# Optimization experiments

Measured on AMD Instinct MI355X. Metric: run time of the kernel, lower is better.

## Reference

```python
import jax, jax.numpy as jnp
import numpy as np

N = 100000      # num_nodes
E = 1600000     # num_edges (avg degree 16)
IN = 128        # in_channels
HID = 8         # hidden_channels (per head)
HEADS = 8
OUT = 64        # out_channels
NEG_SLOPE = 0.2


def setup_inputs() -> dict:
    key = jax.random.key(0)
    ks = jax.random.split(key, 11)
    s = 0.05
    return {
        "x": jax.random.normal(ks[0], (N, IN), jnp.float32),
        "edge_index": jax.random.randint(ks[1], (2, E), 0, N, dtype=jnp.int32),
        "W1": jax.random.normal(ks[2], (IN, HEADS * HID), jnp.float32) * s,
        "a_src1": jax.random.normal(ks[3], (HEADS, HID), jnp.float32) * s,
        "a_dst1": jax.random.normal(ks[4], (HEADS, HID), jnp.float32) * s,
        "b1": jnp.zeros((HEADS * HID,), jnp.float32),
        "W2": jax.random.normal(ks[5], (HEADS * HID, OUT), jnp.float32) * s,
        "a_src2": jax.random.normal(ks[6], (1, OUT), jnp.float32) * s,
        "a_dst2": jax.random.normal(ks[7], (1, OUT), jnp.float32) * s,
        "b2": jnp.zeros((OUT,), jnp.float32),
    }


def gat_conv(x, src, dst, W, a_src, a_dst, bias, heads, out_ch):
    """PyG GATConv (concat=True, dropout=0, self-loops already in src/dst)."""
    n = x.shape[0]
    h = (x @ W).reshape(n, heads, out_ch)               # [N, H, C]
    al_src = jnp.einsum('nhc,hc->nh', h, a_src)          # [N, H]
    al_dst = jnp.einsum('nhc,hc->nh', h, a_dst)          # [N, H]
    e = jax.nn.leaky_relu(al_src[src] + al_dst[dst], NEG_SLOPE)  # [E, H]
    # segment softmax over destination nodes (numerically stable)
    e_max = jax.ops.segment_max(e, dst, num_segments=n)  # [N, H]
    ex = jnp.exp(e - e_max[dst])
    denom = jax.ops.segment_sum(ex, dst, num_segments=n)
    alpha = ex / (denom[dst] + 1e-16)                    # [E, H]
    msg = h[src] * alpha[:, :, None]                     # [E, H, C]
    out = jax.ops.segment_sum(msg, dst, num_segments=n)  # [N, H, C]
    return out.reshape(n, heads * out_ch) + bias


def reference(x, edge_index, W1, a_src1, a_dst1, b1, W2, a_src2, a_dst2, b2):
    n = x.shape[0]
    loops = jnp.arange(n, dtype=edge_index.dtype)
    src = jnp.concatenate([edge_index[0], loops])        # add self-loops (PyG default)
    dst = jnp.concatenate([edge_index[1], loops])
    h = gat_conv(x, src, dst, W1, a_src1, a_dst1, b1, HEADS, HID)
    h = jax.nn.elu(h)
    out = gat_conv(h, src, dst, W2, a_src2, a_dst2, b2, 1, OUT)
    return out
```

## Files before the change

kernel.cpp:

```cpp
#include <hip/hip_runtime.h>
#include <hip/hip_bf16.h>

#define IN_CH   128
#define HEADS   8
#define HID     8
#define MID_CH  64
#define OUT_CH  64
#define CAP     64
#define NRANGE  8
#define NFILLB  256

typedef unsigned short u16;
__device__ __forceinline__ u16 f2bu(float f) {
    union { float f; unsigned int i; } v; v.f = f;
    unsigned int lsb = (v.i >> 16) & 1u;
    return (u16)((v.i + 0x7fffu + lsb) >> 16);
}
__device__ __forceinline__ float2 up2(unsigned int u) {
    union { unsigned int i; float f; } a, b;
    a.i = u << 16; b.i = u & 0xffff0000u;
    return make_float2(a.f, b.f);
}
__device__ __forceinline__ float lrelu(float e) { return (e > 0.f) ? e : 0.2f * e; }

#define FILL_ISSUE(U, D4, S4, P4)                                              \
    do {                                                                        \
        int range_ = (U) & (NRANGE - 1);                                        \
        int chunk_ = (U) >> 3;                                                  \
        int lo_ = (int)(((long long)N * range_) >> 3);                          \
        int hi_ = (int)(((long long)N * (range_ + 1)) >> 3);                    \
        int base_ = (chunk_ * 256 + threadIdx.x) * 4;                           \
        if (base_ + 3 < E) {                                                    \
            D4 = *(const int4*)(dst + base_);                                   \
            bool ix_ = (D4.x >= lo_ && D4.x < hi_);                             \
            bool iy_ = (D4.y >= lo_ && D4.y < hi_);                             \
            bool iz_ = (D4.z >= lo_ && D4.z < hi_);                             \
            bool iw_ = (D4.w >= lo_ && D4.w < hi_);                             \
            if (ix_ | iy_ | iz_ | iw_) {                                        \
                S4 = *(const int4*)(src + base_);                               \
                if (ix_) P4.x = atomicAdd(&deg[D4.x], 1);                       \
                if (iy_) P4.y = atomicAdd(&deg[D4.y], 1);                       \
                if (iz_) P4.z = atomicAdd(&deg[D4.z], 1);                       \
                if (iw_) P4.w = atomicAdd(&deg[D4.w], 1);                       \
            }                                                                   \
        } else {                                                                \
            for (int j_ = 0; j_ < 4; j_++) {                                    \
                int e_ = base_ + j_;                                            \
                if (e_ < E) {                                                   \
                    int d_ = dst[e_];                                           \
                    if (d_ >= lo_ && d_ < hi_) {                                \
                        int p_ = atomicAdd(&deg[d_], 1);                        \
                        if (p_ < CAP) adj[(size_t)d_ * CAP + p_] = src[e_];     \
                    }                                                           \
                }                                                               \
            }                                                                   \
        }                                                                       \
    } while (0)

#define FILL_STORE(D4, S4, P4)                                                  \
    do {                                                                        \
        if (P4.x < CAP) adj[(size_t)D4.x * CAP + P4.x] = S4.x;                  \
        if (P4.y < CAP) adj[(size_t)D4.y * CAP + P4.y] = S4.y;                  \
        if (P4.z < CAP) adj[(size_t)D4.z * CAP + P4.z] = S4.z;                  \
        if (P4.w < CAP) adj[(size_t)D4.w * CAP + P4.w] = S4.w;                  \
    } while (0)

__global__ __launch_bounds__(256, 4) void k12_roles(
    const int* __restrict__ src, const int* __restrict__ dst,
    int* __restrict__ deg, int* __restrict__ adj,
    const float* __restrict__ x, const float* __restrict__ W1,
    const float* __restrict__ a_src, const float* __restrict__ a_dst,
    u16* __restrict__ h1b, float* __restrict__ als, float* __restrict__ ald,
    int E, int N)
{
    __shared__ float Wl[IN_CH * MID_CH];
    __shared__ float xl[16 * IN_CH];
    int bid = blockIdx.x;
    int tid = threadIdx.x;

    if (bid < NFILLB) {
        int range = bid & 7;
        int cstart = bid >> 3;
        int chunks = (E + 1023) >> 10;
        for (int c = cstart; c < chunks; c += 128) {
            int4 dA = make_int4(0,0,0,0), sA = make_int4(0,0,0,0);
            int4 pA = make_int4(CAP,CAP,CAP,CAP);
            int4 dB = make_int4(0,0,0,0), sB = make_int4(0,0,0,0);
            int4 pB = make_int4(CAP,CAP,CAP,CAP);
            int4 dC = make_int4(0,0,0,0), sC = make_int4(0,0,0,0);
            int4 pC = make_int4(CAP,CAP,CAP,CAP);
            int4 dD = make_int4(0,0,0,0), sD = make_int4(0,0,0,0);
            int4 pD = make_int4(CAP,CAP,CAP,CAP);
            FILL_ISSUE(c * 8 + range, dA, sA, pA);
            if (c +  32 < chunks) { int u_ = (c +  32) * 8 + range; FILL_ISSUE(u_, dB, sB, pB); }
            if (c +  64 < chunks) { int u_ = (c +  64) * 8 + range; FILL_ISSUE(u_, dC, sC, pC); }
            if (c +  96 < chunks) { int u_ = (c +  96) * 8 + range; FILL_ISSUE(u_, dD, sD, pD); }
            FILL_STORE(dA, sA, pA);
            FILL_STORE(dB, sB, pB);
            FILL_STORE(dC, sC, pC);
            FILL_STORE(dD, sD, pD);
        }
        return;
    }

    int gid = bid - NFILLB;
    {
        const float4* W4 = (const float4*)W1;
        float4* Wl4 = (float4*)Wl;
        #pragma unroll
        for (int i = tid; i < IN_CH * MID_CH / 4; i += 256) Wl4[i] = W4[i];
    }
    int base = gid * 16;
    {
        float4* xl4 = (float4*)xl;
        const float4* x4 = (const float4*)x;
        #pragma unroll
        for (int i = tid; i < 16 * IN_CH / 4; i += 256) {
            int r = i >> 5;
            int n = base + r;
            xl4[i] = (n < N) ? x4[(size_t)n * (IN_CH / 4) + (i & 31)]
                             : make_float4(0.f, 0.f, 0.f, 0.f);
        }
    }
    __syncthreads();

    int wave = tid >> 6, lane = tid & 63;
    int r0 = wave * 4;
    const float* xr0 = &xl[(r0 + 0) * IN_CH];
    const float* xr1 = &xl[(r0 + 1) * IN_CH];
    const float* xr2 = &xl[(r0 + 2) * IN_CH];
    const float* xr3 = &xl[(r0 + 3) * IN_CH];
    float acc0 = 0.f, acc1 = 0.f, acc2 = 0.f, acc3 = 0.f;
    #pragma unroll 8
    for (int kc = 0; kc < IN_CH; kc += 4) {
        float4 xa = *(const float4*)(xr0 + kc);
        float4 xb = *(const float4*)(xr1 + kc);
        float4 xc = *(const float4*)(xr2 + kc);
        float4 xd = *(const float4*)(xr3 + kc);
        float w0 = Wl[(kc + 0) * MID_CH + lane];
        float w1 = Wl[(kc + 1) * MID_CH + lane];
        float w2 = Wl[(kc + 2) * MID_CH + lane];
        float w3 = Wl[(kc + 3) * MID_CH + lane];
        acc0 = fmaf(xa.x, w0, acc0); acc0 = fmaf(xa.y, w1, acc0);
        acc0 = fmaf(xa.z, w2, acc0); acc0 = fmaf(xa.w, w3, acc0);
        acc1 = fmaf(xb.x, w0, acc1); acc1 = fmaf(xb.y, w1, acc1);
        acc1 = fmaf(xb.z, w2, acc1); acc1 = fmaf(xb.w, w3, acc1);
        acc2 = fmaf(xc.x, w0, acc2); acc2 = fmaf(xc.y, w1, acc2);
        acc2 = fmaf(xc.z, w2, acc2); acc2 = fmaf(xc.w, w3, acc2);
        acc3 = fmaf(xd.x, w0, acc3); acc3 = fmaf(xd.y, w1, acc3);
        acc3 = fmaf(xd.z, w2, acc3); acc3 = fmaf(xd.w, w3, acc3);
    }
    float accs[4] = {acc0, acc1, acc2, acc3};
    float asv = a_src[lane];
    float adv = a_dst[lane];
    #pragma unroll
    for (int g = 0; g < 4; g++) {
        int n = base + r0 + g;
        if (n >= N) continue;
        h1b[(size_t)n * MID_CH + lane] = f2bu(accs[g]);
        float vs = accs[g] * asv;
        float vd = accs[g] * adv;
        vs += __shfl_xor(vs, 1); vs += __shfl_xor(vs, 2); vs += __shfl_xor(vs, 4);
        vd += __shfl_xor(vd, 1); vd += __shfl_xor(vd, 2); vd += __shfl_xor(vd, 4);
        if ((lane & 7) == 0) {
            als[n * HEADS + (lane >> 3)] = vs;
            ald[n * HEADS + (lane >> 3)] = vd;
        }
    }
}

__global__ __launch_bounds__(256) void k34_agg1gemm2(
    const int* __restrict__ deg, const int* __restrict__ adj,
    const u16* __restrict__ h1b, const float* __restrict__ als,
    const float* __restrict__ ald, const float* __restrict__ b1,
    const float* __restrict__ W2, const float* __restrict__ as2,
    const float* __restrict__ ad2,
    u16* __restrict__ t2b, float* __restrict__ als2, float* __restrict__ ald2,
    int N)
{
    __shared__ int adjl[4][CAP];
    __shared__ float h2l[4][MID_CH];
    int tid = threadIdx.x;
    int wave = tid >> 6, lane = tid & 63;
    int n = blockIdx.x * 4 + wave;
    bool valid = (n < N);
    int nc = valid ? n : (N - 1);

    int g = lane >> 3;
    int c8 = lane & 7;
    int dg = deg[nc]; if (dg > CAP) dg = CAP;
    if (lane < dg) adjl[wave][lane] = adj[(size_t)nc * CAP + lane];
    float aldv = ald[nc * HEADS + c8];
    __syncthreads();

    const uint4* h1v = (const uint4*)h1b;
    float acc[8] = {0,0,0,0,0,0,0,0};
    float denom = 0.f;
    for (int i = g; i < dg; i += 8) {
        int s = adjl[wave][i];
        float ex = __expf(lrelu(als[s * HEADS + c8] + aldv));
        uint4 q = h1v[(size_t)s * 8 + c8];
        float2 p0 = up2(q.x), p1 = up2(q.y), p2 = up2(q.z), p3 = up2(q.w);
        denom += ex;
        acc[0] += ex * p0.x; acc[1] += ex * p0.y;
        acc[2] += ex * p1.x; acc[3] += ex * p1.y;
        acc[4] += ex * p2.x; acc[5] += ex * p2.y;
        acc[6] += ex * p3.x; acc[7] += ex * p3.y;
    }
    if (g == 0) {
        float ex = __expf(lrelu(als[nc * HEADS + c8] + aldv));
        uint4 q = h1v[(size_t)nc * 8 + c8];
        float2 p0 = up2(q.x), p1 = up2(q.y), p2 = up2(q.z), p3 = up2(q.w);
        denom += ex;
        acc[0] += ex * p0.x; acc[1] += ex * p0.y;
        acc[2] += ex * p1.x; acc[3] += ex * p1.y;
        acc[4] += ex * p2.x; acc[5] += ex * p2.y;
        acc[6] += ex * p3.x; acc[7] += ex * p3.y;
    }
    denom += __shfl_xor(denom, 8); denom += __shfl_xor(denom, 16); denom += __shfl_xor(denom, 32);
    #pragma unroll
    for (int j = 0; j < 8; j++) {
        acc[j] += __shfl_xor(acc[j], 8);
        acc[j] += __shfl_xor(acc[j], 16);
        acc[j] += __shfl_xor(acc[j], 32);
    }
    float inv = 1.f / (denom + 1e-16f);

    if (g == 0 && valid) {
        const float4* b4 = (const float4*)b1;
        float4 bl = b4[c8 * 2], bh = b4[c8 * 2 + 1];
        float4 o0, o1;
        o0.x = acc[0] * inv + bl.x; o0.y = acc[1] * inv + bl.y;
        o0.z = acc[2] * inv + bl.z; o0.w = acc[3] * inv + bl.w;
        o1.x = acc[4] * inv + bh.x; o1.y = acc[5] * inv + bh.y;
        o1.z = acc[6] * inv + bh.z; o1.w = acc[7] * inv + bh.w;
        o0.x = (o0.x > 0.f) ? o0.x : (__expf(o0.x) - 1.f);
        o0.y = (o0.y > 0.f) ? o0.y : (__expf(o0.y) - 1.f);
        o0.z = (o0.z > 0.f) ? o0.z : (__expf(o0.z) - 1.f);
        o0.w = (o0.w > 0.f) ? o0.w : (__expf(o0.w) - 1.f);
        o1.x = (o1.x > 0.f) ? o1.x : (__expf(o1.x) - 1.f);
        o1.y = (o1.y > 0.f) ? o1.y : (__expf(o1.y) - 1.f);
        o1.z = (o1.z > 0.f) ? o1.z : (__expf(o1.z) - 1.f);
        o1.w = (o1.w > 0.f) ? o1.w : (__expf(o1.w) - 1.f);
        float4* h2v = (float4*)h2l[wave];
        h2v[c8 * 2]     = o0;
        h2v[c8 * 2 + 1] = o1;
    }
    __syncthreads();

    const float* hr = h2l[wave];
    float acc2 = 0.f;
    #pragma unroll 8
    for (int kc = 0; kc < MID_CH; kc += 4) {
        float4 hv = *(const float4*)(hr + kc);
        float w0 = W2[(kc + 0) * OUT_CH + lane];
        float w1 = W2[(kc + 1) * OUT_CH + lane];
        float w2 = W2[(kc + 2) * OUT_CH + lane];
        float w3 = W2[(kc + 3) * OUT_CH + lane];
        acc2 = fmaf(hv.x, w0, acc2); acc2 = fmaf(hv.y, w1, acc2);
        acc2 = fmaf(hv.z, w2, acc2); acc2 = fmaf(hv.w, w3, acc2);
    }
    if (valid) {
        t2b[(size_t)n * OUT_CH + lane] = f2bu(acc2);
        float vs = acc2 * as2[lane];
        float vd = acc2 * ad2[lane];
        #pragma unroll
        for (int off = 1; off < 64; off <<= 1) {
            vs += __shfl_xor(vs, off);
            vd += __shfl_xor(vd, off);
        }
        if (lane == 0) { als2[n] = vs; ald2[n] = vd; }
    }
}

__global__ __launch_bounds__(256) void k5_agg2(
    const int* __restrict__ deg, const int* __restrict__ adj,
    const u16* __restrict__ t2b, const float* __restrict__ als,
    const float* __restrict__ ald, const float* __restrict__ b2,
    float* __restrict__ out, int N)
{
    __shared__ int adjl[4][CAP];
    int wave = threadIdx.x >> 6, lane = threadIdx.x & 63;
    int n = blockIdx.x * 4 + wave;
    bool valid = (n < N);
    int nc = valid ? n : (N - 1);

    int g = lane >> 3;
    int c8 = lane & 7;
    int dg = deg[nc]; if (dg > CAP) dg = CAP;
    if (lane < dg) adjl[wave][lane] = adj[(size_t)nc * CAP + lane];
    float aldv = ald[nc];
    __syncthreads();

    const uint4* t2v = (const uint4*)t2b;
    float acc[8] = {0,0,0,0,0,0,0,0};
    float denom = 0.f;
    for (int i = g; i < dg; i += 8) {
        int s = adjl[wave][i];
        float ex = __expf(lrelu(als[s] + aldv));
        uint4 q = t2v[(size_t)s * 8 + c8];
        float2 p0 = up2(q.x), p1 = up2(q.y), p2 = up2(q.z), p3 = up2(q.w);
        denom += ex;
        acc[0] += ex * p0.x; acc[1] += ex * p0.y;
        acc[2] += ex * p1.x; acc[3] += ex * p1.y;
        acc[4] += ex * p2.x; acc[5] += ex * p2.y;
        acc[6] += ex * p3.x; acc[7] += ex * p3.y;
    }
    if (g == 0) {
        float ex = __expf(lrelu(als[nc] + aldv));
        uint4 q = t2v[(size_t)nc * 8 + c8];
        float2 p0 = up2(q.x), p1 = up2(q.y), p2 = up2(q.z), p3 = up2(q.w);
        denom += ex;
        acc[0] += ex * p0.x; acc[1] += ex * p0.y;
        acc[2] += ex * p1.x; acc[3] += ex * p1.y;
        acc[4] += ex * p2.x; acc[5] += ex * p2.y;
        acc[6] += ex * p3.x; acc[7] += ex * p3.y;
    }
    denom += __shfl_xor(denom, 8); denom += __shfl_xor(denom, 16); denom += __shfl_xor(denom, 32);
    #pragma unroll
    for (int j = 0; j < 8; j++) {
        acc[j] += __shfl_xor(acc[j], 8);
        acc[j] += __shfl_xor(acc[j], 16);
        acc[j] += __shfl_xor(acc[j], 32);
    }
    float inv = 1.f / (denom + 1e-16f);

    if (g == 0 && valid) {
        const float4* b4 = (const float4*)b2;
        float4 bl = b4[c8 * 2], bh = b4[c8 * 2 + 1];
        float4 o0, o1;
        o0.x = acc[0] * inv + bl.x; o0.y = acc[1] * inv + bl.y;
        o0.z = acc[2] * inv + bl.z; o0.w = acc[3] * inv + bl.w;
        o1.x = acc[4] * inv + bh.x; o1.y = acc[5] * inv + bh.y;
        o1.z = acc[6] * inv + bh.z; o1.w = acc[7] * inv + bh.w;
        float4* ov = (float4*)out;
        ov[(size_t)n * 16 + c8 * 2]     = o0;
        ov[(size_t)n * 16 + c8 * 2 + 1] = o1;
    }
}

extern "C" void kernel_launch(void* const* d_in, const int* in_sizes, int n_in,
                              void* d_out, int out_size, void* d_ws, size_t ws_size,
                              hipStream_t stream) {
    const float* x   = (const float*)d_in[0];
    const int*   ei  = (const int*)d_in[1];
    const float* W1  = (const float*)d_in[2];
    const float* as1 = (const float*)d_in[3];
    const float* ad1 = (const float*)d_in[4];
    const float* b1  = (const float*)d_in[5];
    const float* W2  = (const float*)d_in[6];
    const float* as2 = (const float*)d_in[7];
    const float* ad2 = (const float*)d_in[8];
    const float* b2  = (const float*)d_in[9];
    float* out = (float*)d_out;

    int N = in_sizes[0] / IN_CH;
    int E = in_sizes[1] / 2;
    const int* srcp = ei;
    const int* dstp = ei + E;

    char* w = (char*)d_ws;
    size_t off = 0;
    auto alloc = [&](size_t bytes) {
        void* p = w + off;
        off += (bytes + 255) & ~(size_t)255;
        return p;
    };
    int*   deg  = (int*)  alloc((size_t)N * 4);
    int*   adj  = (int*)  alloc((size_t)N * CAP * 4);
    u16*   h1b  = (u16*)  alloc((size_t)N * MID_CH * 2);
    float* als1 = (float*)alloc((size_t)N * HEADS * 4);
    float* ald1 = (float*)alloc((size_t)N * HEADS * 4);
    u16*   t2b  = (u16*)  alloc((size_t)N * OUT_CH * 2);
    float* als2 = (float*)alloc((size_t)N * 4);
    float* ald2 = (float*)alloc((size_t)N * 4);
    (void)ws_size; (void)n_in; (void)out_size;

    hipMemsetAsync(deg, 0, (size_t)N * 4, stream);

    int ngemm = (N + 15) / 16;
    k12_roles<<<NFILLB + ngemm, 256, 0, stream>>>(srcp, dstp, deg, adj,
                                                  x, W1, as1, ad1, h1b, als1, ald1,
                                                  E, N);
    k34_agg1gemm2<<<(N + 3) / 4, 256, 0, stream>>>(deg, adj, h1b, als1, ald1, b1,
                                                   W2, as2, ad2, t2b, als2, ald2, N);
    k5_agg2<<<(N + 3) / 4, 256, 0, stream>>>(deg, adj, t2b, als2, ald2, b2, out, N);
}
```

Before: 348.6 us.

## Replace global-atomic adjacency fill with two-pass bucketed counting sort

The single-pass fill, which scanned every edge eight times (once per destination range) and did a global atomic per edge, is replaced. The first pass bins each edge by destination block of 256 nodes, using shared-memory histograms plus one global atomic per bucket, and writes (src,dst) pairs to a staging buffer. A new kernel then builds each bucket's adjacency lists with shared-memory atomics and writes the degrees directly. This removes the repeated edge reads and the global atomic contention, at the cost of an extra kernel launch and a staging round trip through memory. Buckets are capped at 6144 edges, so a heavily skewed graph could silently drop edges.

```diff
diff --git a/kernel.cpp b/kernel.cpp
--- a/kernel.cpp
+++ b/kernel.cpp
@@ -7,8 +7,8 @@
 #define MID_CH  64
 #define OUT_CH  64
 #define CAP     64
-#define NRANGE  8
-#define NFILLB  256
+#define NPB     256
+#define CAPB    6144
 
 typedef unsigned short u16;
 __device__ __forceinline__ u16 f2bu(float f) {
@@ -23,87 +23,86 @@
 }
 __device__ __forceinline__ float lrelu(float e) { return (e > 0.f) ? e : 0.2f * e; }
 
-#define FILL_ISSUE(U, D4, S4, P4)                                              \
-    do {                                                                        \
-        int range_ = (U) & (NRANGE - 1);                                        \
-        int chunk_ = (U) >> 3;                                                  \
-        int lo_ = (int)(((long long)N * range_) >> 3);                          \
-        int hi_ = (int)(((long long)N * (range_ + 1)) >> 3);                    \
-        int base_ = (chunk_ * 256 + threadIdx.x) * 4;                           \
-        if (base_ + 3 < E) {                                                    \
-            D4 = *(const int4*)(dst + base_);                                   \
-            bool ix_ = (D4.x >= lo_ && D4.x < hi_);                             \
-            bool iy_ = (D4.y >= lo_ && D4.y < hi_);                             \
-            bool iz_ = (D4.z >= lo_ && D4.z < hi_);                             \
-            bool iw_ = (D4.w >= lo_ && D4.w < hi_);                             \
-            if (ix_ | iy_ | iz_ | iw_) {                                        \
-                S4 = *(const int4*)(src + base_);                               \
-                if (ix_) P4.x = atomicAdd(&deg[D4.x], 1);                       \
-                if (iy_) P4.y = atomicAdd(&deg[D4.y], 1);                       \
-                if (iz_) P4.z = atomicAdd(&deg[D4.z], 1);                       \
-                if (iw_) P4.w = atomicAdd(&deg[D4.w], 1);                       \
-            }                                                                   \
-        } else {                                                                \
-            for (int j_ = 0; j_ < 4; j_++) {                                    \
-                int e_ = base_ + j_;                                            \
-                if (e_ < E) {                                                   \
-                    int d_ = dst[e_];                                           \
-                    if (d_ >= lo_ && d_ < hi_) {                                \
-                        int p_ = atomicAdd(&deg[d_], 1);                        \
-                        if (p_ < CAP) adj[(size_t)d_ * CAP + p_] = src[e_];     \
-                    }                                                           \
-                }                                                               \
-            }                                                                   \
-        }                                                                       \
-    } while (0)
-
-#define FILL_STORE(D4, S4, P4)                                                  \
-    do {                                                                        \
-        if (P4.x < CAP) adj[(size_t)D4.x * CAP + P4.x] = S4.x;                  \
-        if (P4.y < CAP) adj[(size_t)D4.y * CAP + P4.y] = S4.y;                  \
-        if (P4.z < CAP) adj[(size_t)D4.z * CAP + P4.z] = S4.z;                  \
-        if (P4.w < CAP) adj[(size_t)D4.w * CAP + P4.w] = S4.w;                  \
-    } while (0)
-
-__global__ __launch_bounds__(256, 4) void k12_roles(
+__global__ __launch_bounds__(256, 4) void kA_bucket_gemm(
     const int* __restrict__ src, const int* __restrict__ dst,
-    int* __restrict__ deg, int* __restrict__ adj,
+    int* __restrict__ fillc, int2* __restrict__ stg,
     const float* __restrict__ x, const float* __restrict__ W1,
     const float* __restrict__ a_src, const float* __restrict__ a_dst,
     u16* __restrict__ h1b, float* __restrict__ als, float* __restrict__ ald,
-    int E, int N)
+    int E, int N, int NB, int nFillA)
 {
-    __shared__ float Wl[IN_CH * MID_CH];
-    __shared__ float xl[16 * IN_CH];
+    __shared__ __align__(16) char smem[40960];
     int bid = blockIdx.x;
     int tid = threadIdx.x;
 
-    if (bid < NFILLB) {
-        int range = bid & 7;
-        int cstart = bid >> 3;
-        int chunks = (E + 1023) >> 10;
-        for (int c = cstart; c < chunks; c += 128) {
-            int4 dA = make_int4(0,0,0,0), sA = make_int4(0,0,0,0);
-            int4 pA = make_int4(CAP,CAP,CAP,CAP);
-            int4 dB = make_int4(0,0,0,0), sB = make_int4(0,0,0,0);
-            int4 pB = make_int4(CAP,CAP,CAP,CAP);
-            int4 dC = make_int4(0,0,0,0), sC = make_int4(0,0,0,0);
-            int4 pC = make_int4(CAP,CAP,CAP,CAP);
-            int4 dD = make_int4(0,0,0,0), sD = make_int4(0,0,0,0);
-            int4 pD = make_int4(CAP,CAP,CAP,CAP);
-            FILL_ISSUE(c * 8 + range, dA, sA, pA);
-            if (c +  32 < chunks) { int u_ = (c +  32) * 8 + range; FILL_ISSUE(u_, dB, sB, pB); }
-            if (c +  64 < chunks) { int u_ = (c +  64) * 8 + range; FILL_ISSUE(u_, dC, sC, pC); }
-            if (c +  96 < chunks) { int u_ = (c +  96) * 8 + range; FILL_ISSUE(u_, dD, sD, pD); }
-            FILL_STORE(dA, sA, pA);
-            FILL_STORE(dB, sB, pB);
-            FILL_STORE(dC, sC, pC);
-            FILL_STORE(dD, sD, pD);
+    if (bid < nFillA) {
+        int* cnt   = (int*)smem;
+        int* basel = cnt + 512;
+        for (int i = tid; i < NB; i += 256) cnt[i] = 0;
+        __syncthreads();
+
+        int eA = bid * 2048 + tid * 4;
+        int eB = eA + 1024;
+        int4 dA = make_int4(0,0,0,0), dB = make_int4(0,0,0,0);
+        bool vA = (eA + 3 < E), vB = (eB + 3 < E);
+        if (vA) {
+            dA = *(const int4*)(dst + eA);
+            atomicAdd(&cnt[dA.x >> 8], 1);
+            atomicAdd(&cnt[dA.y >> 8], 1);
+            atomicAdd(&cnt[dA.z >> 8], 1);
+            atomicAdd(&cnt[dA.w >> 8], 1);
+        } else {
+            for (int j = 0; j < 4; j++) { int e = eA + j; if (e < E) atomicAdd(&cnt[dst[e] >> 8], 1); }
+        }
+        if (vB) {
+            dB = *(const int4*)(dst + eB);
+            atomicAdd(&cnt[dB.x >> 8], 1);
+            atomicAdd(&cnt[dB.y >> 8], 1);
+            atomicAdd(&cnt[dB.z >> 8], 1);
+            atomicAdd(&cnt[dB.w >> 8], 1);
+        } else {
+            for (int j = 0; j < 4; j++) { int e = eB + j; if (e < E) atomicAdd(&cnt[dst[e] >> 8], 1); }
+        }
+        __syncthreads();
+
+        for (int i = tid; i < NB; i += 256) {
+            int c = cnt[i];
+            int idx = i * CAPB;
+            if (c > 0) idx += atomicAdd(&fillc[i], c);
+            basel[i] = idx;
+        }
+        __syncthreads();
+
+        if (vA) {
+            int4 sA = *(const int4*)(src + eA);
+            int b0 = dA.x >> 8; int p0 = atomicAdd(&basel[b0], 1); if (p0 < (b0 + 1) * CAPB) stg[p0] = make_int2(sA.x, dA.x);
+            int b1 = dA.y >> 8; int p1 = atomicAdd(&basel[b1], 1); if (p1 < (b1 + 1) * CAPB) stg[p1] = make_int2(sA.y, dA.y);
+            int b2 = dA.z >> 8; int p2 = atomicAdd(&basel[b2], 1); if (p2 < (b2 + 1) * CAPB) stg[p2] = make_int2(sA.z, dA.z);
+            int b3 = dA.w >> 8; int p3 = atomicAdd(&basel[b3], 1); if (p3 < (b3 + 1) * CAPB) stg[p3] = make_int2(sA.w, dA.w);
+        } else {
+            for (int j = 0; j < 4; j++) {
+                int e = eA + j;
+                if (e < E) { int d = dst[e]; int b = d >> 8; int p = atomicAdd(&basel[b], 1); if (p < (b + 1) * CAPB) stg[p] = make_int2(src[e], d); }
+            }
+        }
+        if (vB) {
+            int4 sB = *(const int4*)(src + eB);
+            int b0 = dB.x >> 8; int p0 = atomicAdd(&basel[b0], 1); if (p0 < (b0 + 1) * CAPB) stg[p0] = make_int2(sB.x, dB.x);
+            int b1 = dB.y >> 8; int p1 = atomicAdd(&basel[b1], 1); if (p1 < (b1 + 1) * CAPB) stg[p1] = make_int2(sB.y, dB.y);
+            int b2 = dB.z >> 8; int p2 = atomicAdd(&basel[b2], 1); if (p2 < (b2 + 1) * CAPB) stg[p2] = make_int2(sB.z, dB.z);
+            int b3 = dB.w >> 8; int p3 = atomicAdd(&basel[b3], 1); if (p3 < (b3 + 1) * CAPB) stg[p3] = make_int2(sB.w, dB.w);
+        } else {
+            for (int j = 0; j < 4; j++) {
+                int e = eB + j;
+                if (e < E) { int d = dst[e]; int b = d >> 8; int p = atomicAdd(&basel[b], 1); if (p < (b + 1) * CAPB) stg[p] = make_int2(src[e], d); }
+            }
         }
         return;
     }
 
-    int gid = bid - NFILLB;
+    float* Wl = (float*)smem;
+    float* xl = (float*)(smem + 32768);
+    int gid = bid - nFillA;
     {
         const float4* W4 = (const float4*)W1;
         float4* Wl4 = (float4*)Wl;
@@ -169,6 +168,30 @@
     }
 }
 
+__global__ __launch_bounds__(256) void kD_build(
+    const int2* __restrict__ stg, const int* __restrict__ fillc,
+    int* __restrict__ deg, int* __restrict__ adj, int N)
+{
+    __shared__ int dl[NPB];
+    int b = blockIdx.x;
+    int tid = threadIdx.x;
+    int lo = b * NPB;
+    dl[tid] = 0;
+    __syncthreads();
+
+    int cntb = fillc[b];
+    if (cntb > CAPB) cntb = CAPB;
+    const int2* sp = stg + (size_t)b * CAPB;
+    for (int i = tid; i < cntb; i += 256) {
+        int2 p = sp[i];
+        int slot = atomicAdd(&dl[p.y - lo], 1);
+        if (slot < CAP) adj[(size_t)p.y * CAP + slot] = p.x;
+    }
+    __syncthreads();
+    int n = lo + tid;
+    if (n < N) deg[n] = dl[tid];
+}
+
 __global__ __launch_bounds__(256) void k34_agg1gemm2(
     const int* __restrict__ deg, const int* __restrict__ adj,
     const u16* __restrict__ h1b, const float* __restrict__ als,
@@ -359,6 +382,8 @@
     const int* srcp = ei;
     const int* dstp = ei + E;
 
+    int NB = (N + NPB - 1) / NPB;
+
     char* w = (char*)d_ws;
     size_t off = 0;
     auto alloc = [&](size_t bytes) {
@@ -374,14 +399,19 @@
     u16*   t2b  = (u16*)  alloc((size_t)N * OUT_CH * 2);
     float* als2 = (float*)alloc((size_t)N * 4);
     float* ald2 = (float*)alloc((size_t)N * 4);
+    int2*  stg  = (int2*) alloc((size_t)NB * CAPB * 8);
+    int*   filc = (int*)  alloc((size_t)NB * 4);
     (void)ws_size; (void)n_in; (void)out_size;
 
-    hipMemsetAsync(deg, 0, (size_t)N * 4, stream);
-
-    int ngemm = (N + 15) / 16;
-    k12_roles<<<NFILLB + ngemm, 256, 0, stream>>>(srcp, dstp, deg, adj,
-                                                  x, W1, as1, ad1, h1b, als1, ald1,
-                                                  E, N);
+    hipMemsetAsync(filc, 0, (size_t)NB * 4, stream);
+
+    int nFillA = (E + 2047) / 2048;
+    int ngemm  = (N + 15) / 16;
+    kA_bucket_gemm<<<nFillA + ngemm, 256, 0, stream>>>(srcp, dstp, filc, stg,
+                                                       x, W1, as1, ad1,
+                                                       h1b, als1, ald1,
+                                                       E, N, NB, nFillA);
+    kD_build<<<NB, 256, 0, stream>>>(stg, filc, deg, adj, N);
     k34_agg1gemm2<<<(N + 3) / 4, 256, 0, stream>>>(deg, adj, h1b, als1, ald1, b1,
                                                    W2, as2, ad2, t2b, als2, ald2, N);
     k5_agg2<<<(N + 3) / 4, 256, 0, stream>>>(deg, adj, t2b, als2, ald2, b2, out, N);
```

Measured after the change: 348.2 us. No clear change (-0.1%).
